# Optimization experiments

Hardware: AMD Instinct MI355X
Metric: run time of the kernel (lower is better)

## Reference

```python
import jax, jax.numpy as jnp
import numpy as np

B, H, S, D = 2, 16, 2048, 64
DEGREE = 2
EPS = 1e-4


def setup_inputs() -> dict:
    key = jax.random.key(0)
    kq, kk, kv = jax.random.split(key, 3)
    q = jax.random.normal(kq, (B, H, S, D), dtype=jnp.float32)
    k = jax.random.normal(kk, (B, H, S, D), dtype=jnp.float32)
    v = jax.random.normal(kv, (B, H, S, D), dtype=jnp.float32)
    return {"q": q, "k": k, "v": v}


def reference(q, k, v):
    # dots: [B,H,S,S] = QK^T
    dots = jnp.einsum("bhsd,bhtd->bhst", q, k)
    # polynomial kernel: x^degree, row-normalized with clamped denom
    x = dots ** DEGREE
    denom = jnp.maximum(x.sum(axis=-1, keepdims=True), EPS)
    attn = x / denom
    # weighted V sum: [B,H,S,D]
    return jnp.einsum("bhst,bhtd->bhsd", attn, v)
```

## Files before the change

### kernel.cpp

```cpp
#include <hip/hip_runtime.h>


#define S_LEN 2048
#define DH    64
#define BQ    64
#define BK    64
#define LSTR  72
#define EPSTR 68
#define PSTR  65
#define BH_N  32
#define PER_BH (S_LEN * DH)
#define NT    (S_LEN / BK)

typedef __bf16 bf16x8 __attribute__((ext_vector_type(8)));
typedef __bf16 bf16x2 __attribute__((ext_vector_type(2)));
typedef float  f32x4  __attribute__((ext_vector_type(4)));
typedef float  f32x16 __attribute__((ext_vector_type(16)));
typedef unsigned int uivec2 __attribute__((ext_vector_type(2)));

__device__ __forceinline__ unsigned short f2bf(float f) {
    union { float f; unsigned int u; } x; x.f = f;
    unsigned int u = x.u;
    return (unsigned short)((u + 0x7fffu + ((u >> 16) & 1u)) >> 16);
}

__device__ __forceinline__ unsigned int pack2bf(float lo, float hi) {
#if __has_builtin(__builtin_amdgcn_cvt_pk_bf16_f32)
    bf16x2 p = __builtin_amdgcn_cvt_pk_bf16_f32(lo, hi);
    union { bf16x2 v; unsigned int u; } c; c.v = p;
    return c.u;
#else
    return (unsigned int)f2bf(lo) | ((unsigned int)f2bf(hi) << 16);
#endif
}

__device__ __forceinline__ void pl32swap(unsigned int& a, unsigned int& b) {
#if __has_builtin(__builtin_amdgcn_permlane32_swap)
    uivec2 r = __builtin_amdgcn_permlane32_swap(a, b, false, false);
    a = r[0]; b = r[1];
#else
    asm("v_permlane32_swap_b32 %0, %1" : "+v"(a), "+v"(b));
#endif
}

__global__ __launch_bounds__(256)
void prepass_kernel(const float* __restrict__ kg, const float* __restrict__ vg,
                    unsigned short* __restrict__ kbf, unsigned short* __restrict__ vt)
{
    __shared__ unsigned short Ls[64 * PSTR];
    const int tid = threadIdx.x;
    const int bh  = blockIdx.y;
    const int t0  = blockIdx.x * 64;
    const size_t base = (size_t)bh * PER_BH + (size_t)t0 * DH;

    {
        const float4* src = (const float4*)(kg + base + (size_t)tid * 16);
        float4 a = src[0], b = src[1], c = src[2], d = src[3];
        union { unsigned short h[8]; uint4 v; } u0, u1;
        u0.h[0]=f2bf(a.x); u0.h[1]=f2bf(a.y); u0.h[2]=f2bf(a.z); u0.h[3]=f2bf(a.w);
        u0.h[4]=f2bf(b.x); u0.h[5]=f2bf(b.y); u0.h[6]=f2bf(b.z); u0.h[7]=f2bf(b.w);
        u1.h[0]=f2bf(c.x); u1.h[1]=f2bf(c.y); u1.h[2]=f2bf(c.z); u1.h[3]=f2bf(c.w);
        u1.h[4]=f2bf(d.x); u1.h[5]=f2bf(d.y); u1.h[6]=f2bf(d.z); u1.h[7]=f2bf(d.w);
        uint4* dst = (uint4*)(kbf + base + (size_t)tid * 16);
        dst[0] = u0.v; dst[1] = u1.v;
    }

    const float* vb = vg + base;
    #pragma unroll
    for (int r = 0; r < 4; ++r) {
        int idx = r * 256 + tid;
        int row = idx >> 4, c4 = idx & 15;
        float4 f = ((const float4*)vb)[idx];
        unsigned short* p = &Ls[row * PSTR + c4 * 4];
        p[0] = f2bf(f.x); p[1] = f2bf(f.y); p[2] = f2bf(f.z); p[3] = f2bf(f.w);
    }
    __syncthreads();
    #pragma unroll
    for (int r = 0; r < 2; ++r) {
        int idx = r * 256 + tid;
        int d = idx >> 3, j8 = idx & 7;
        union { unsigned short h[8]; uint4 v; } u;
        #pragma unroll
        for (int jj = 0; jj < 8; ++jj) u.h[jj] = Ls[(j8 * 8 + jj) * PSTR + d];
        *(uint4*)(vt + (size_t)bh * PER_BH + (size_t)d * S_LEN + t0 + j8 * 8) = u.v;
    }
}

__global__ __launch_bounds__(256, 4)
void poly_attn_main(const float* __restrict__ qg,
                    const unsigned short* __restrict__ kbf,
                    const unsigned short* __restrict__ vtbf,
                    float* __restrict__ og)
{
    __shared__ __align__(16) unsigned short smem[4 * 64 * LSTR];
    __shared__ float dbuf[128];
    #define KS_BASE(b)  ((b) * 64 * LSTR)
    #define VTS_BASE(b) ((2 + (b)) * 64 * LSTR)

    const int tid  = threadIdx.x;
    const int lane = tid & 63;
    const int w    = tid >> 6;
    const int p    = w >> 1;
    const int e    = w & 1;
    const int l31  = lane & 31;
    const int h    = lane >> 5;

    const int bh = blockIdx.y;
    const int q0 = blockIdx.x * BQ;

    const float* qb = qg + ((size_t)bh * S_LEN + q0) * DH;
    const unsigned short* kb  = kbf  + (size_t)bh * PER_BH;
    const unsigned short* vtb = vtbf + (size_t)bh * PER_BH;
    float* ob = og + ((size_t)bh * S_LEN + q0) * DH;

    bf16x8 qfrag[4];
    #pragma unroll
    for (int ks = 0; ks < 4; ++ks) {
        const float* qp = qb + (32 * p + l31) * DH + ks * 16 + h * 8;
        float4 f0 = *(const float4*)qp;
        float4 f1 = *(const float4*)(qp + 4);
        union { unsigned int d[4]; bf16x8 v; } u;
        u.d[0] = pack2bf(f0.x, f0.y);
        u.d[1] = pack2bf(f0.z, f0.w);
        u.d[2] = pack2bf(f1.x, f1.y);
        u.d[3] = pack2bf(f1.z, f1.w);
        qfrag[ks] = u.v;
    }

    f32x16 oacc[2];
    #pragma unroll
    for (int mt = 0; mt < 2; ++mt)
        #pragma unroll
        for (int r = 0; r < 16; ++r) oacc[mt][r] = 0.f;
    float dsum = 0.f;

    const int srow = tid >> 3;
    const int sc8  = tid & 7;

    uint4 kreg[2], vreg[2];
    #pragma unroll
    for (int it = 0; it < 2; ++it) {
        int row = srow + it * 32;
        kreg[it] = *(const uint4*)(kb + (size_t)row * DH + sc8 * 8);
        vreg[it] = *(const uint4*)(vtb + (size_t)row * S_LEN + sc8 * 8);
    }
    #pragma unroll
    for (int it = 0; it < 2; ++it) {
        int row = srow + it * 32;
        *(uint4*)&smem[KS_BASE(0)  + row * LSTR + sc8 * 8] = kreg[it];
        *(uint4*)&smem[VTS_BASE(0) + row * LSTR + sc8 * 8] = vreg[it];
    }
    __syncthreads();

    for (int t = 0; t < NT; ++t) {
        const int cur = t & 1;
        if (t + 1 < NT) {
            const int t0n = (t + 1) * BK;
            #pragma unroll
            for (int it = 0; it < 2; ++it) {
                int row = srow + it * 32;
                kreg[it] = *(const uint4*)(kb + (size_t)(t0n + row) * DH + sc8 * 8);
                vreg[it] = *(const uint4*)(vtb + (size_t)row * S_LEN + t0n + sc8 * 8);
            }
        }

        f32x16 acc;
        #pragma unroll
        for (int r = 0; r < 16; ++r) acc[r] = 0.f;
        #pragma unroll
        for (int ks = 0; ks < 4; ++ks) {
            bf16x8 kf = *(const bf16x8*)&smem[KS_BASE(cur) + (e * 32 + l31) * LSTR + ks * 16 + h * 8];
            acc = __builtin_amdgcn_mfma_f32_32x32x16_bf16(kf, qfrag[ks], acc, 0, 0, 0);
        }

        unsigned int pk[4][2];
        #pragma unroll
        for (int g = 0; g < 4; ++g) {
            float x0 = acc[4*g+0], x1 = acc[4*g+1], x2 = acc[4*g+2], x3 = acc[4*g+3];
            x0 *= x0; x1 *= x1; x2 *= x2; x3 *= x3;
            dsum += (x0 + x1) + (x2 + x3);
            pk[g][0] = pack2bf(x0, x1);
            pk[g][1] = pack2bf(x2, x3);
        }
        unsigned int bfrag[2][4];
        #pragma unroll
        for (int ksl = 0; ksl < 2; ++ksl) {
            unsigned int a0 = pk[2*ksl][0], b0 = pk[2*ksl+1][0];
            unsigned int a1 = pk[2*ksl][1], b1 = pk[2*ksl+1][1];
            pl32swap(a0, b0);
            pl32swap(a1, b1);
            bfrag[ksl][0] = a0; bfrag[ksl][1] = a1;
            bfrag[ksl][2] = b0; bfrag[ksl][3] = b1;
        }

        #pragma unroll
        for (int mt = 0; mt < 2; ++mt) {
            #pragma unroll
            for (int ksl = 0; ksl < 2; ++ksl) {
                bf16x8 vf = *(const bf16x8*)&smem[VTS_BASE(cur) + (mt * 32 + l31) * LSTR + e * 32 + ksl * 16 + h * 8];
                union { unsigned int d[4]; bf16x8 v; } u;
                u.d[0] = bfrag[ksl][0]; u.d[1] = bfrag[ksl][1];
                u.d[2] = bfrag[ksl][2]; u.d[3] = bfrag[ksl][3];
                oacc[mt] = __builtin_amdgcn_mfma_f32_32x32x16_bf16(vf, u.v, oacc[mt], 0, 0, 0);
            }
        }

        if (t + 1 < NT) {
            #pragma unroll
            for (int it = 0; it < 2; ++it) {
                int row = srow + it * 32;
                *(uint4*)&smem[KS_BASE(cur ^ 1)  + row * LSTR + sc8 * 8] = kreg[it];
                *(uint4*)&smem[VTS_BASE(cur ^ 1) + row * LSTR + sc8 * 8] = vreg[it];
            }
            __syncthreads();
        }
    }

    float wavetot = dsum + __shfl_xor(dsum, 32);

    __syncthreads();
    float* ep = (float*)smem + (size_t)w * (32 * EPSTR);
    #pragma unroll
    for (int mt = 0; mt < 2; ++mt) {
        #pragma unroll
        for (int g = 0; g < 4; ++g) {
            f32x4 vv;
            vv[0] = oacc[mt][4*g+0];
            vv[1] = oacc[mt][4*g+1];
            vv[2] = oacc[mt][4*g+2];
            vv[3] = oacc[mt][4*g+3];
            *(f32x4*)&ep[l31 * EPSTR + mt * 32 + 8 * g + 4 * h] = vv;
        }
    }
    if (h == 0) dbuf[w * 32 + l31] = wavetot;
    __syncthreads();

    const float* ep0 = (float*)smem + (size_t)(2 * p)     * (32 * EPSTR);
    const float* ep1 = (float*)smem + (size_t)(2 * p + 1) * (32 * EPSTR);
    const int lrow = e * 16 + (lane >> 2);
    const float den = dbuf[2 * p * 32 + lrow] + dbuf[(2 * p + 1) * 32 + lrow];
    const float inv = 1.0f / fmaxf(den, 1e-4f);
    #pragma unroll
    for (int it = 0; it < 4; ++it) {
        int d0 = (lane & 3) * 16 + it * 4;
        f32x4 a = *(const f32x4*)&ep0[lrow * EPSTR + d0];
        f32x4 b = *(const f32x4*)&ep1[lrow * EPSTR + d0];
        f32x4 s;
        s[0] = (a[0] + b[0]) * inv;
        s[1] = (a[1] + b[1]) * inv;
        s[2] = (a[2] + b[2]) * inv;
        s[3] = (a[3] + b[3]) * inv;
        *(f32x4*)&ob[(32 * p + lrow) * DH + d0] = s;
    }
    #undef KS_BASE
    #undef VTS_BASE
}

__global__ __launch_bounds__(256, 2)
void poly_attn_fallback(const float* __restrict__ qg, const float* __restrict__ kg,
                        const float* __restrict__ vg, float* __restrict__ og)
{
    __shared__ unsigned short Qs[64 * LSTR];
    __shared__ unsigned short Ksl[64 * LSTR];
    __shared__ unsigned short Vt[64 * LSTR];
    __shared__ unsigned short Xsl[64 * LSTR];

    const int tid  = threadIdx.x;
    const int lane = tid & 63;
    const int w    = tid >> 6;
    const int c    = lane & 15;
    const int quad = lane >> 4;
    const int i0   = w * 16;

    const int bh = blockIdx.y;
    const int q0 = blockIdx.x * 64;

    const float* qb = qg + ((size_t)bh * S_LEN + q0) * DH;
    const float* kb = kg + (size_t)bh * S_LEN * DH;
    const float* vb = vg + (size_t)bh * S_LEN * DH;
    float*       ob = og + ((size_t)bh * S_LEN + q0) * DH;

    {
        const float4* qf4 = (const float4*)qb;
        #pragma unroll
        for (int r = 0; r < 4; ++r) {
            int idx = r * 256 + tid;
            int row = idx >> 4, c4 = idx & 15;
            float4 f = qf4[idx];
            ushort4 hh;
            hh.x = f2bf(f.x); hh.y = f2bf(f.y); hh.z = f2bf(f.z); hh.w = f2bf(f.w);
            *(ushort4*)&Qs[row * LSTR + c4 * 4] = hh;
        }
    }

    f32x4 oacc[4];
    #pragma unroll
    for (int t = 0; t < 4; ++t) { oacc[t][0]=0.f; oacc[t][1]=0.f; oacc[t][2]=0.f; oacc[t][3]=0.f; }
    float dsum[4] = {0.f, 0.f, 0.f, 0.f};

    for (int t0 = 0; t0 < S_LEN; t0 += 64) {
        __syncthreads();
        {
            const float4* kf4 = (const float4*)(kb + (size_t)t0 * DH);
            const float4* vf4 = (const float4*)(vb + (size_t)t0 * DH);
            #pragma unroll
            for (int r = 0; r < 4; ++r) {
                int idx = r * 256 + tid;
                int row = idx >> 4, c4 = idx & 15;
                float4 f = kf4[idx];
                ushort4 hh;
                hh.x = f2bf(f.x); hh.y = f2bf(f.y); hh.z = f2bf(f.z); hh.w = f2bf(f.w);
                *(ushort4*)&Ksl[row * LSTR + c4 * 4] = hh;
                float4 g = vf4[idx];
                int d0 = c4 * 4;
                Vt[(d0 + 0) * LSTR + row] = f2bf(g.x);
                Vt[(d0 + 1) * LSTR + row] = f2bf(g.y);
                Vt[(d0 + 2) * LSTR + row] = f2bf(g.z);
                Vt[(d0 + 3) * LSTR + row] = f2bf(g.w);
            }
        }
        __syncthreads();

        f32x4 xacc[4];
        #pragma unroll
        for (int t = 0; t < 4; ++t) { xacc[t][0]=0.f; xacc[t][1]=0.f; xacc[t][2]=0.f; xacc[t][3]=0.f; }
        #pragma unroll
        for (int k0 = 0; k0 < 64; k0 += 32) {
            bf16x8 af = *(const bf16x8*)&Qs[(i0 + c) * LSTR + k0 + quad * 8];
            #pragma unroll
            for (int tn = 0; tn < 4; ++tn) {
                bf16x8 bfg = *(const bf16x8*)&Ksl[(tn * 16 + c) * LSTR + k0 + quad * 8];
                xacc[tn] = __builtin_amdgcn_mfma_f32_16x16x32_bf16(af, bfg, xacc[tn], 0, 0, 0);
            }
        }
        #pragma unroll
        for (int tn = 0; tn < 4; ++tn)
            #pragma unroll
            for (int r = 0; r < 4; ++r) {
                float xv = xacc[tn][r];
                float xs = xv * xv;
                dsum[r] += xs;
                Xsl[(i0 + quad * 4 + r) * LSTR + tn * 16 + c] = f2bf(xs);
            }
        __syncthreads();

        #pragma unroll
        for (int k0 = 0; k0 < 64; k0 += 32) {
            bf16x8 af = *(const bf16x8*)&Xsl[(i0 + c) * LSTR + k0 + quad * 8];
            #pragma unroll
            for (int tn = 0; tn < 4; ++tn) {
                bf16x8 bfg = *(const bf16x8*)&Vt[(tn * 16 + c) * LSTR + k0 + quad * 8];
                oacc[tn] = __builtin_amdgcn_mfma_f32_16x16x32_bf16(af, bfg, oacc[tn], 0, 0, 0);
            }
        }
    }

    #pragma unroll
    for (int r = 0; r < 4; ++r) {
        float s = dsum[r];
        s += __shfl_xor(s, 1);
        s += __shfl_xor(s, 2);
        s += __shfl_xor(s, 4);
        s += __shfl_xor(s, 8);
        dsum[r] = 1.0f / fmaxf(s, 1e-4f);
    }
    #pragma unroll
    for (int tn = 0; tn < 4; ++tn)
        #pragma unroll
        for (int r = 0; r < 4; ++r)
            ob[(i0 + quad * 4 + r) * DH + tn * 16 + c] = oacc[tn][r] * dsum[r];
}

extern "C" void kernel_launch(void* const* d_in, const int* in_sizes, int n_in,
                              void* d_out, int out_size, void* d_ws, size_t ws_size,
                              hipStream_t stream) {
    (void)in_sizes; (void)n_in; (void)out_size;
    const float* q = (const float*)d_in[0];
    const float* k = (const float*)d_in[1];
    const float* v = (const float*)d_in[2];
    float* o = (float*)d_out;

    const size_t elems = (size_t)BH_N * PER_BH;
    const size_t need  = 2 * elems * sizeof(unsigned short);

    if (ws_size >= need) {
        unsigned short* kbf = (unsigned short*)d_ws;
        unsigned short* vtb = kbf + elems;
        prepass_kernel<<<dim3(S_LEN / 64, BH_N), 256, 0, stream>>>(k, v, kbf, vtb);
        poly_attn_main<<<dim3(S_LEN / BQ, BH_N), 256, 0, stream>>>(q, kbf, vtb, o);
    } else {
        poly_attn_fallback<<<dim3(S_LEN / 64, BH_N), 256, 0, stream>>>(q, k, v, o);
    }
}
```

Before: 155.5 us.

## Pre-swizzle K/V into MFMA fragment order and load straight to registers

The prepass now writes bf16 K and V in the exact per-lane MFMA fragment order. The main kernel can then fetch each tile's operands with coalesced 16-byte global loads straight into registers, dropping the LDS double buffer and the per-tile __syncthreads. K is software-pipelined one tile ahead in registers across a manually unrolled pair of tiles. The grid is flattened and remapped so neighbouring blocks cover different batch-heads, for better cache spreading. The trade-off is that waves sharing the same K/V now each reload them through the caches instead of sharing one LDS copy, and more registers are needed to hold the tile buffers.

```diff
diff --git a/kernel.cpp b/kernel.cpp
--- a/kernel.cpp
+++ b/kernel.cpp
@@ -5,7 +5,6 @@
 #define DH    64
 #define BQ    64
 #define BK    64
-#define LSTR  72
 #define EPSTR 68
 #define PSTR  65
 #define BH_N  32
@@ -45,57 +44,65 @@
 
 __global__ __launch_bounds__(256)
 void prepass_kernel(const float* __restrict__ kg, const float* __restrict__ vg,
-                    unsigned short* __restrict__ kbf, unsigned short* __restrict__ vt)
+                    unsigned short* __restrict__ kfo, unsigned short* __restrict__ vfo)
 {
-    __shared__ unsigned short Ls[64 * PSTR];
+    __shared__ unsigned short Lk[64 * 72];
+    __shared__ unsigned short Lv[64 * PSTR];
     const int tid = threadIdx.x;
     const int bh  = blockIdx.y;
-    const int t0  = blockIdx.x * 64;
-    const size_t base = (size_t)bh * PER_BH + (size_t)t0 * DH;
-
-    {
-        const float4* src = (const float4*)(kg + base + (size_t)tid * 16);
-        float4 a = src[0], b = src[1], c = src[2], d = src[3];
-        union { unsigned short h[8]; uint4 v; } u0, u1;
-        u0.h[0]=f2bf(a.x); u0.h[1]=f2bf(a.y); u0.h[2]=f2bf(a.z); u0.h[3]=f2bf(a.w);
-        u0.h[4]=f2bf(b.x); u0.h[5]=f2bf(b.y); u0.h[6]=f2bf(b.z); u0.h[7]=f2bf(b.w);
-        u1.h[0]=f2bf(c.x); u1.h[1]=f2bf(c.y); u1.h[2]=f2bf(c.z); u1.h[3]=f2bf(c.w);
-        u1.h[4]=f2bf(d.x); u1.h[5]=f2bf(d.y); u1.h[6]=f2bf(d.z); u1.h[7]=f2bf(d.w);
-        uint4* dst = (uint4*)(kbf + base + (size_t)tid * 16);
-        dst[0] = u0.v; dst[1] = u1.v;
-    }
-
-    const float* vb = vg + base;
+    const int t   = blockIdx.x;
+    const size_t base = (size_t)bh * PER_BH + (size_t)t * 64 * DH;
+
+    const float4* kf4 = (const float4*)(kg + base);
+    const float4* vf4 = (const float4*)(vg + base);
     #pragma unroll
     for (int r = 0; r < 4; ++r) {
         int idx = r * 256 + tid;
         int row = idx >> 4, c4 = idx & 15;
-        float4 f = ((const float4*)vb)[idx];
-        unsigned short* p = &Ls[row * PSTR + c4 * 4];
-        p[0] = f2bf(f.x); p[1] = f2bf(f.y); p[2] = f2bf(f.z); p[3] = f2bf(f.w);
+        float4 f = kf4[idx];
+        ushort4 hh;
+        hh.x = f2bf(f.x); hh.y = f2bf(f.y); hh.z = f2bf(f.z); hh.w = f2bf(f.w);
+        *(ushort4*)&Lk[row * 72 + c4 * 4] = hh;
+        float4 g = vf4[idx];
+        unsigned short* pv = &Lv[row * PSTR + c4 * 4];
+        pv[0] = f2bf(g.x); pv[1] = f2bf(g.y); pv[2] = f2bf(g.z); pv[3] = f2bf(g.w);
     }
     __syncthreads();
+
+    unsigned short* kout = kfo + (size_t)bh * PER_BH + (size_t)t * 4096;
     #pragma unroll
     for (int r = 0; r < 2; ++r) {
-        int idx = r * 256 + tid;
-        int d = idx >> 3, j8 = idx & 7;
-        union { unsigned short h[8]; uint4 v; } u;
-        #pragma unroll
-        for (int jj = 0; jj < 8; ++jj) u.h[jj] = Ls[(j8 * 8 + jj) * PSTR + d];
-        *(uint4*)(vt + (size_t)bh * PER_BH + (size_t)d * S_LEN + t0 + j8 * 8) = u.v;
+        int pos = r * 256 + tid;
+        int lam = pos & 63, rest = pos >> 6;
+        int e = rest >> 2, ks = rest & 3;
+        int l31 = lam & 31, h = lam >> 5;
+        uint4 v = *(const uint4*)&Lk[(e * 32 + l31) * 72 + ks * 16 + h * 8];
+        *(uint4*)(kout + (size_t)pos * 8) = v;
+    }
+    unsigned short* vout = vfo + (size_t)bh * PER_BH + (size_t)t * 4096;
+    #pragma unroll
+    for (int r = 0; r < 2; ++r) {
+        int pos = r * 256 + tid;
+        int lam = pos & 63, rest = pos >> 6;
+        int e = rest >> 2, ksl = (rest >> 1) & 1, mt = rest & 1;
+        int l31 = lam & 31, h = lam >> 5;
+        int d  = mt * 32 + l31;
+        int j0 = e * 32 + ksl * 16 + h * 8;
+        union { unsigned short s[8]; uint4 u; } u;
+        #pragma unroll
+        for (int jj = 0; jj < 8; ++jj) u.s[jj] = Lv[(j0 + jj) * PSTR + d];
+        *(uint4*)(vout + (size_t)pos * 8) = u.u;
     }
 }
 
 __global__ __launch_bounds__(256, 4)
 void poly_attn_main(const float* __restrict__ qg,
-                    const unsigned short* __restrict__ kbf,
-                    const unsigned short* __restrict__ vtbf,
+                    const unsigned short* __restrict__ kfo,
+                    const unsigned short* __restrict__ vfo,
                     float* __restrict__ og)
 {
-    __shared__ __align__(16) unsigned short smem[4 * 64 * LSTR];
+    __shared__ float epb[4 * 32 * EPSTR];
     __shared__ float dbuf[128];
-    #define KS_BASE(b)  ((b) * 64 * LSTR)
-    #define VTS_BASE(b) ((2 + (b)) * 64 * LSTR)
 
     const int tid  = threadIdx.x;
     const int lane = tid & 63;
@@ -105,12 +112,14 @@
     const int l31  = lane & 31;
     const int h    = lane >> 5;
 
-    const int bh = blockIdx.y;
-    const int q0 = blockIdx.x * BQ;
+    const int id = blockIdx.x;
+    const int bh = (id & 7) * 4 + ((id >> 3) & 3);
+    const int qt = id >> 5;
+    const int q0 = qt * BQ;
 
     const float* qb = qg + ((size_t)bh * S_LEN + q0) * DH;
-    const unsigned short* kb  = kbf  + (size_t)bh * PER_BH;
-    const unsigned short* vtb = vtbf + (size_t)bh * PER_BH;
+    const unsigned short* kw = kfo + (size_t)bh * PER_BH + e * 2048 + (size_t)lane * 8;
+    const unsigned short* vw = vfo + (size_t)bh * PER_BH + e * 2048 + (size_t)lane * 8;
     float* ob = og + ((size_t)bh * S_LEN + q0) * DH;
 
     bf16x8 qfrag[4];
@@ -134,92 +143,63 @@
         for (int r = 0; r < 16; ++r) oacc[mt][r] = 0.f;
     float dsum = 0.f;
 
-    const int srow = tid >> 3;
-    const int sc8  = tid & 7;
-
-    uint4 kreg[2], vreg[2];
-    #pragma unroll
-    for (int it = 0; it < 2; ++it) {
-        int row = srow + it * 32;
-        kreg[it] = *(const uint4*)(kb + (size_t)row * DH + sc8 * 8);
-        vreg[it] = *(const uint4*)(vtb + (size_t)row * S_LEN + sc8 * 8);
-    }
-    #pragma unroll
-    for (int it = 0; it < 2; ++it) {
-        int row = srow + it * 32;
-        *(uint4*)&smem[KS_BASE(0)  + row * LSTR + sc8 * 8] = kreg[it];
-        *(uint4*)&smem[VTS_BASE(0) + row * LSTR + sc8 * 8] = vreg[it];
-    }
-    __syncthreads();
-
-    for (int t = 0; t < NT; ++t) {
-        const int cur = t & 1;
-        if (t + 1 < NT) {
-            const int t0n = (t + 1) * BK;
-            #pragma unroll
-            for (int it = 0; it < 2; ++it) {
-                int row = srow + it * 32;
-                kreg[it] = *(const uint4*)(kb + (size_t)(t0n + row) * DH + sc8 * 8);
-                vreg[it] = *(const uint4*)(vtb + (size_t)row * S_LEN + t0n + sc8 * 8);
-            }
-        }
-
-        f32x16 acc;
-        #pragma unroll
-        for (int r = 0; r < 16; ++r) acc[r] = 0.f;
-        #pragma unroll
-        for (int ks = 0; ks < 4; ++ks) {
-            bf16x8 kf = *(const bf16x8*)&smem[KS_BASE(cur) + (e * 32 + l31) * LSTR + ks * 16 + h * 8];
-            acc = __builtin_amdgcn_mfma_f32_32x32x16_bf16(kf, qfrag[ks], acc, 0, 0, 0);
-        }
-
-        unsigned int pk[4][2];
-        #pragma unroll
-        for (int g = 0; g < 4; ++g) {
-            float x0 = acc[4*g+0], x1 = acc[4*g+1], x2 = acc[4*g+2], x3 = acc[4*g+3];
-            x0 *= x0; x1 *= x1; x2 *= x2; x3 *= x3;
-            dsum += (x0 + x1) + (x2 + x3);
-            pk[g][0] = pack2bf(x0, x1);
-            pk[g][1] = pack2bf(x2, x3);
-        }
-        unsigned int bfrag[2][4];
-        #pragma unroll
-        for (int ksl = 0; ksl < 2; ++ksl) {
-            unsigned int a0 = pk[2*ksl][0], b0 = pk[2*ksl+1][0];
-            unsigned int a1 = pk[2*ksl][1], b1 = pk[2*ksl+1][1];
-            pl32swap(a0, b0);
-            pl32swap(a1, b1);
-            bfrag[ksl][0] = a0; bfrag[ksl][1] = a1;
-            bfrag[ksl][2] = b0; bfrag[ksl][3] = b1;
-        }
-
-        #pragma unroll
-        for (int mt = 0; mt < 2; ++mt) {
-            #pragma unroll
-            for (int ksl = 0; ksl < 2; ++ksl) {
-                bf16x8 vf = *(const bf16x8*)&smem[VTS_BASE(cur) + (mt * 32 + l31) * LSTR + e * 32 + ksl * 16 + h * 8];
-                union { unsigned int d[4]; bf16x8 v; } u;
-                u.d[0] = bfrag[ksl][0]; u.d[1] = bfrag[ksl][1];
-                u.d[2] = bfrag[ksl][2]; u.d[3] = bfrag[ksl][3];
-                oacc[mt] = __builtin_amdgcn_mfma_f32_32x32x16_bf16(vf, u.v, oacc[mt], 0, 0, 0);
-            }
-        }
-
-        if (t + 1 < NT) {
-            #pragma unroll
-            for (int it = 0; it < 2; ++it) {
-                int row = srow + it * 32;
-                *(uint4*)&smem[KS_BASE(cur ^ 1)  + row * LSTR + sc8 * 8] = kreg[it];
-                *(uint4*)&smem[VTS_BASE(cur ^ 1) + row * LSTR + sc8 * 8] = vreg[it];
-            }
-            __syncthreads();
-        }
-    }
+    uint4 kbuf[2][4], vbuf[4];
+    #pragma unroll
+    for (int ks = 0; ks < 4; ++ks)
+        kbuf[0][ks] = *(const uint4*)(kw + ks * 512);
+
+#define TILE_BODY(T, KCUR, KNXT)                                                    \
+    {                                                                               \
+        const unsigned short* vt_ = vw + (size_t)(T) * 4096;                        \
+        _Pragma("unroll")                                                           \
+        for (int x = 0; x < 4; ++x)                                                 \
+            vbuf[x] = *(const uint4*)(vt_ + x * 512);                               \
+        f32x16 acc;                                                                 \
+        _Pragma("unroll")                                                           \
+        for (int r = 0; r < 16; ++r) acc[r] = 0.f;                                  \
+        _Pragma("unroll")                                                           \
+        for (int ks = 0; ks < 4; ++ks) {                                            \
+            union { uint4 u; bf16x8 v; } kc; kc.u = KCUR[ks];                       \
+            acc = __builtin_amdgcn_mfma_f32_32x32x16_bf16(kc.v, qfrag[ks], acc, 0, 0, 0); \
+        }                                                                           \
+        const unsigned short* kn_ = kw + (size_t)((T) + 1) * 4096;                  \
+        _Pragma("unroll")                                                           \
+        for (int ks = 0; ks < 4; ++ks)                                              \
+            KNXT[ks] = *(const uint4*)(kn_ + ks * 512);                             \
+        unsigned int pk[4][2];                                                      \
+        _Pragma("unroll")                                                           \
+        for (int g = 0; g < 4; ++g) {                                               \
+            float x0 = acc[4*g+0], x1 = acc[4*g+1], x2 = acc[4*g+2], x3 = acc[4*g+3]; \
+            x0 *= x0; x1 *= x1; x2 *= x2; x3 *= x3;                                 \
+            dsum += (x0 + x1) + (x2 + x3);                                          \
+            pk[g][0] = pack2bf(x0, x1);                                             \
+            pk[g][1] = pack2bf(x2, x3);                                             \
+        }                                                                           \
+        _Pragma("unroll")                                                           \
+        for (int ksl = 0; ksl < 2; ++ksl) {                                         \
+            unsigned int a0 = pk[2*ksl][0], b0 = pk[2*ksl+1][0];                    \
+            unsigned int a1 = pk[2*ksl][1], b1 = pk[2*ksl+1][1];                    \
+            pl32swap(a0, b0);                                                       \
+            pl32swap(a1, b1);                                                       \
+            union { unsigned int d[4]; bf16x8 v; } bu;                              \
+            bu.d[0] = a0; bu.d[1] = a1; bu.d[2] = b0; bu.d[3] = b1;                 \
+            _Pragma("unroll")                                                       \
+            for (int mt = 0; mt < 2; ++mt) {                                        \
+                union { uint4 u; bf16x8 v; } vv; vv.u = vbuf[ksl * 2 + mt];         \
+                oacc[mt] = __builtin_amdgcn_mfma_f32_32x32x16_bf16(vv.v, bu.v, oacc[mt], 0, 0, 0); \
+            }                                                                       \
+        }                                                                           \
+    }
+
+    for (int tp = 0; tp < NT; tp += 2) {
+        TILE_BODY(tp,     kbuf[0], kbuf[1]);
+        TILE_BODY(tp + 1, kbuf[1], kbuf[0]);
+    }
+#undef TILE_BODY
 
     float wavetot = dsum + __shfl_xor(dsum, 32);
 
-    __syncthreads();
-    float* ep = (float*)smem + (size_t)w * (32 * EPSTR);
+    float* ep = epb + (size_t)w * (32 * EPSTR);
     #pragma unroll
     for (int mt = 0; mt < 2; ++mt) {
         #pragma unroll
@@ -235,8 +215,8 @@
     if (h == 0) dbuf[w * 32 + l31] = wavetot;
     __syncthreads();
 
-    const float* ep0 = (float*)smem + (size_t)(2 * p)     * (32 * EPSTR);
-    const float* ep1 = (float*)smem + (size_t)(2 * p + 1) * (32 * EPSTR);
+    const float* ep0 = epb + (size_t)(2 * p)     * (32 * EPSTR);
+    const float* ep1 = epb + (size_t)(2 * p + 1) * (32 * EPSTR);
     const int lrow = e * 16 + (lane >> 2);
     const float den = dbuf[2 * p * 32 + lrow] + dbuf[(2 * p + 1) * 32 + lrow];
     const float inv = 1.0f / fmaxf(den, 1e-4f);
@@ -252,10 +232,9 @@
         s[3] = (a[3] + b[3]) * inv;
         *(f32x4*)&ob[(32 * p + lrow) * DH + d0] = s;
     }
-    #undef KS_BASE
-    #undef VTS_BASE
-}
-
+}
+
+#define LSTR 72
 __global__ __launch_bounds__(256, 2)
 void poly_attn_fallback(const float* __restrict__ qg, const float* __restrict__ kg,
                         const float* __restrict__ vg, float* __restrict__ og)
@@ -384,10 +363,10 @@
     const size_t need  = 2 * elems * sizeof(unsigned short);
 
     if (ws_size >= need) {
-        unsigned short* kbf = (unsigned short*)d_ws;
-        unsigned short* vtb = kbf + elems;
-        prepass_kernel<<<dim3(S_LEN / 64, BH_N), 256, 0, stream>>>(k, v, kbf, vtb);
-        poly_attn_main<<<dim3(S_LEN / BQ, BH_N), 256, 0, stream>>>(q, kbf, vtb, o);
+        unsigned short* kfo = (unsigned short*)d_ws;
+        unsigned short* vfo = kfo + elems;
+        prepass_kernel<<<dim3(NT, BH_N), 256, 0, stream>>>(k, v, kfo, vfo);
+        poly_attn_main<<<dim3(BH_N * S_LEN / BQ), 256, 0, stream>>>(q, kfo, vfo, o);
     } else {
         poly_attn_fallback<<<dim3(S_LEN / 64, BH_N), 256, 0, stream>>>(q, k, v, o);
     }
```

Result: faster. 145.8 us (-6.2%).
